# Kernel optimization log

Hardware: AMD Instinct MI355X
Metric: run time of the kernel (lower is better)

## Reference

```python
import jax, jax.numpy as jnp
import numpy as np

B, S, H = 32, 512, 768          # batch, encoder seq len, hidden size
W, G = 128, 4                   # max words per example, max tokens per word group
NH, HD, FF, NL, NLAB = 4, 192, 2048, 2, 6  # heads, head dim, ffn dim, layers, labels
EPS = 1e-5


def setup_inputs() -> dict:
    key = jax.random.key(0)
    ks = jax.random.split(key, 16)
    s = 0.02
    hidden = jax.random.normal(ks[0], (B, S, H), jnp.float32)
    word_token_idx = jax.random.randint(ks[1], (B, W, G), 0, S).astype(jnp.int32)
    glen = jax.random.randint(ks[2], (B, W), 1, G + 1)
    group_token_mask = jnp.arange(G)[None, None, :] < glen[:, :, None]  # [B,W,G] bool
    nwords = jax.random.randint(ks[3], (B,), W // 2, W + 1)
    word_valid = jnp.arange(W)[None, :] < nwords[:, None]               # [B,W] bool
    return {
        'hidden': hidden,
        'word_token_idx': word_token_idx,
        'group_token_mask': group_token_mask,
        'word_valid': word_valid,
        'qkv_w': jax.random.normal(ks[4], (NL, 3 * H, H), jnp.float32) * s,
        'qkv_b': jnp.zeros((NL, 3 * H), jnp.float32),
        'out_w': jax.random.normal(ks[5], (NL, H, H), jnp.float32) * s,
        'out_b': jnp.zeros((NL, H), jnp.float32),
        'ff1_w': jax.random.normal(ks[6], (NL, FF, H), jnp.float32) * s,
        'ff1_b': jnp.zeros((NL, FF), jnp.float32),
        'ff2_w': jax.random.normal(ks[7], (NL, H, FF), jnp.float32) * s,
        'ff2_b': jnp.zeros((NL, H), jnp.float32),
        'ln1_s': jnp.ones((NL, H), jnp.float32),
        'ln1_b': jnp.zeros((NL, H), jnp.float32),
        'ln2_s': jnp.ones((NL, H), jnp.float32),
        'ln2_b': jnp.zeros((NL, H), jnp.float32),
        'cls_w': jax.random.normal(ks[8], (NLAB, H), jnp.float32) * s,
        'cls_b': jnp.zeros((NLAB,), jnp.float32),
    }


def _ln(x, s, b):
    m = x.mean(-1, keepdims=True)
    v = ((x - m) ** 2).mean(-1, keepdims=True)
    return (x - m) * jax.lax.rsqrt(v + EPS) * s + b


def reference(hidden, word_token_idx, group_token_mask, word_valid,
              qkv_w, qkv_b, out_w, out_b, ff1_w, ff1_b, ff2_w, ff2_b,
              ln1_s, ln1_b, ln2_s, ln2_b, cls_w, cls_b):
    dt = hidden.dtype
    # ragged per-word gather + masked mean over each subword group: [B,W,G,H]
    gathered = jax.vmap(lambda h, i: h[i])(hidden, word_token_idx)
    gm = group_token_mask[..., None].astype(dt)
    wemb = (gathered * gm).sum(2) / jnp.maximum(gm.sum(2), 1.0)   # [B,W,H]
    # invalid (padded) words are zero, matching torch pad_sequence zero-padding
    wemb = wemb * word_valid[..., None].astype(dt)
    cls = hidden[:, 0, :]
    x = jnp.concatenate([cls[:, None, :], wemb], axis=1)          # [B, W+1, H]
    # key padding mask: True = padded position; CLS slot always valid
    pad = jnp.concatenate([jnp.zeros((B, 1), bool), ~word_valid], axis=1)
    neg = jnp.finfo(dt).min
    Lw = W + 1
    scale = 1.0 / np.sqrt(HD)
    for l in range(NL):  # 2 post-norm TransformerEncoder layers
        qkv = x @ qkv_w[l].T + qkv_b[l]
        q, k, v = jnp.split(qkv, 3, axis=-1)
        q = q.reshape(B, Lw, NH, HD).transpose(0, 2, 1, 3)
        k = k.reshape(B, Lw, NH, HD).transpose(0, 2, 1, 3)
        v = v.reshape(B, Lw, NH, HD).transpose(0, 2, 1, 3)
        scores = jnp.einsum('bhqd,bhkd->bhqk', q, k) * scale
        scores = jnp.where(pad[:, None, None, :], neg, scores)
        a = jax.nn.softmax(scores, axis=-1)
        ctx = jnp.einsum('bhqk,bhkd->bhqd', a, v).transpose(0, 2, 1, 3).reshape(B, Lw, H)
        attn = ctx @ out_w[l].T + out_b[l]
        x = _ln(x + attn, ln1_s[l], ln1_b[l])
        h1 = jax.nn.relu(x @ ff1_w[l].T + ff1_b[l])
        x = _ln(x + h1 @ ff2_w[l].T + ff2_b[l], ln2_s[l], ln2_b[l])
    pooled = x[:, 0, :]
    logits = pooled @ cls_w.T + cls_b
    return (logits, pooled)
```

## Files before the change

kernel.cpp:

```cpp
#include <hip/hip_runtime.h>
#include <hip/hip_bf16.h>
#include <math.h>

#define B_  32
#define S_  512
#define H_  768
#define W_  128
#define G_  4
#define LW  129
#define NH_ 4
#define HD_ 192
#define FF_ 2048
#define NL_ 2
#define NLAB_ 6
#define M_   (B_ * LW)
#define MPAD 4224
#define EPS_ 1e-5f
#define SCALE_ 0.07216878364870323f

#define TP 192
#define KP 160
#define KR 144
#define KLD 200

#define QW_SZ (3 * H_ * H_)
#define OW_SZ (H_ * H_)
#define F1_SZ (FF_ * H_)
#define F2_SZ (H_ * FF_)
#define WL_SZ (QW_SZ + OW_SZ + F1_SZ + F2_SZ)

typedef __bf16 bf16_8 __attribute__((ext_vector_type(8)));
typedef float  f32x4  __attribute__((ext_vector_type(4)));
typedef unsigned short ushort8_t __attribute__((ext_vector_type(8)));

__device__ __forceinline__ float b2f(unsigned short u) {
    union { unsigned int i; float f; } c; c.i = ((unsigned int)u) << 16; return c.f;
}
__device__ __forceinline__ unsigned short f2b(float f) {
    union { float f; unsigned int u; } c; c.f = f;
    unsigned int u = c.u;
    return (unsigned short)((u + 0x7FFFu + ((u >> 16) & 1u)) >> 16);
}

__device__ __forceinline__ float wave_sum(float v) {
#pragma unroll
    for (int off = 1; off < 64; off <<= 1) v += __shfl_xor(v, off, 64);
    return v;
}
__device__ __forceinline__ float block_sum(float v, float* red) {
    v = wave_sum(v);
    int wid = threadIdx.x >> 6, lane = threadIdx.x & 63;
    if (lane == 0) red[wid] = v;
    __syncthreads();
    float r = (red[0] + red[1]) + (red[2] + red[3]);
    __syncthreads();
    return r;
}

__global__ __launch_bounds__(256) void build_x_kernel(
    const float* __restrict__ hidden,
    const int*   __restrict__ wti,
    const int*   __restrict__ gmask,
    const int*   __restrict__ wvalid,
    unsigned short* __restrict__ xb)
{
    int t = blockIdx.x;
    int b = blockIdx.y;
    int tid = threadIdx.x;
    if (t >= LW) {
        int pr = M_ + b * 3 + (t - LW);
        size_t xo = (size_t)pr * H_;
#pragma unroll
        for (int i = 0; i < 3; i++) xb[xo + tid + i * 256] = 0;
        return;
    }
    size_t xo = ((size_t)b * LW + t) * H_;
    if (t == 0) {
        const float* src = hidden + (size_t)b * S_ * H_;
#pragma unroll
        for (int i = 0; i < 3; i++) xb[xo + tid + i * 256] = f2b(src[tid + i * 256]);
    } else {
        int w = t - 1;
        int valid = wvalid[b * W_ + w];
        int ids[G_]; float msk[G_]; float cnt = 0.f;
#pragma unroll
        for (int g = 0; g < G_; g++) {
            ids[g] = wti[(b * W_ + w) * G_ + g];
            msk[g] = (gmask[(b * W_ + w) * G_ + g] != 0) ? 1.f : 0.f;
            cnt += msk[g];
        }
        float inv = valid ? (1.f / fmaxf(cnt, 1.f)) : 0.f;
#pragma unroll
        for (int i = 0; i < 3; i++) {
            int c = tid + i * 256;
            float a = 0.f;
#pragma unroll
            for (int g = 0; g < G_; g++)
                a += msk[g] * hidden[((size_t)b * S_ + ids[g]) * H_ + c];
            xb[xo + c] = f2b(a * inv);
        }
    }
}

__global__ __launch_bounds__(256) void cvt_all_kernel(
    const float4* __restrict__ qw, const float4* __restrict__ ow,
    const float4* __restrict__ f1, const float4* __restrict__ f2,
    ushort4* __restrict__ dst)
{
    constexpr int WL4 = WL_SZ / 4;
    int i = blockIdx.x * 256 + threadIdx.x;
    int l = (i < WL4) ? 0 : 1;
    int j = i - l * WL4;
    float4 v;
    if (j < QW_SZ / 4)                          v = qw[l * (QW_SZ / 4) + j];
    else if (j < (QW_SZ + OW_SZ) / 4)           v = ow[l * (OW_SZ / 4) + j - QW_SZ / 4];
    else if (j < (QW_SZ + OW_SZ + F1_SZ) / 4)   v = f1[l * (F1_SZ / 4) + j - (QW_SZ + OW_SZ) / 4];
    else                                        v = f2[l * (F2_SZ / 4) + j - (QW_SZ + OW_SZ + F1_SZ) / 4];
    ushort4 o; o.x = f2b(v.x); o.y = f2b(v.y); o.z = f2b(v.z); o.w = f2b(v.w);
    dst[i] = o;
}

template <int BM, int BN, int BK, int RELU, int OUTBF, int SWZ>
__global__ __launch_bounds__(256) void gemm_mfma(
    const unsigned short* __restrict__ A,
    const unsigned short* __restrict__ Bw,
    const float* __restrict__ bias,
    void* __restrict__ Cout,
    int N, int K)
{
    constexpr int MI  = BM / 32;
    constexpr int NJ  = BN / 32;
    constexpr int CPR = BK / 8;
    constexpr int RPL = 2048 / BK;
    constexpr int SA  = BM * BK / 2048;
    constexpr int SB  = BN * BK / 2048;

    __shared__ __align__(16) unsigned short As[BM * BK];
    __shared__ __align__(16) unsigned short Bs[BN * BK];

    const int tid  = threadIdx.x;
    const int lane = tid & 63;
    const int wid  = tid >> 6;

    int bx = blockIdx.x, by = blockIdx.y;
    if (SWZ) {
        int nx = gridDim.x;
        int total = nx * gridDim.y;
        int id = by * nx + bx;
        int id2 = (id & 7) * (total >> 3) + (id >> 3);
        by = id2 / nx; bx = id2 - by * nx;
    }
    const int bm = by * BM;
    const int bn = bx * BN;

    const int wm = (wid & 1) * (BM / 2);
    const int wn = (wid >> 1) * (BN / 2);
    const int r  = lane & 15;
    const int q8 = lane >> 4;
    const int m8 = r & (CPR - 1);

    const int srow = tid / CPR;
    const int scol = (tid % CPR) ^ (srow & (CPR - 1));
    const unsigned short* Ag = A  + (size_t)(bm + srow) * K + scol * 8;
    const unsigned short* Bg = Bw + (size_t)(bn + srow) * K + scol * 8;

    const bf16_8* Af = (const bf16_8*)As;
    const bf16_8* Bf = (const bf16_8*)Bs;
    int arow[MI], brow[NJ];
#pragma unroll
    for (int i = 0; i < MI; i++) arow[i] = (wm + i * 16 + r) * CPR;
#pragma unroll
    for (int j = 0; j < NJ; j++) brow[j] = (wn + j * 16 + r) * CPR;

    f32x4 acc[MI][NJ];
#pragma unroll
    for (int i = 0; i < MI; i++)
#pragma unroll
        for (int j = 0; j < NJ; j++) acc[i][j] = (f32x4){0.f, 0.f, 0.f, 0.f};

    for (int k0 = 0; k0 < K; k0 += BK) {
#pragma unroll
        for (int s = 0; s < SA; s++)
            __builtin_amdgcn_global_load_lds(
                (const __attribute__((address_space(1))) void*)(Ag + (size_t)(s * RPL) * K + k0),
                (__attribute__((address_space(3))) void*)(As + s * 2048 + tid * 8), 16, 0, 0);
#pragma unroll
        for (int s = 0; s < SB; s++)
            __builtin_amdgcn_global_load_lds(
                (const __attribute__((address_space(1))) void*)(Bg + (size_t)(s * RPL) * K + k0),
                (__attribute__((address_space(3))) void*)(Bs + s * 2048 + tid * 8), 16, 0, 0);
        __syncthreads();
#pragma unroll
        for (int ks = 0; ks < BK / 32; ks++) {
            const int cc = (ks * 4 + q8) ^ m8;
            bf16_8 a[MI], b[NJ];
#pragma unroll
            for (int i = 0; i < MI; i++) a[i] = Af[arow[i] + cc];
#pragma unroll
            for (int j = 0; j < NJ; j++) b[j] = Bf[brow[j] + cc];
#pragma unroll
            for (int i = 0; i < MI; i++)
#pragma unroll
                for (int j = 0; j < NJ; j++)
                    acc[i][j] = __builtin_amdgcn_mfma_f32_16x16x32_bf16(a[i], b[j], acc[i][j], 0, 0, 0);
        }
        __syncthreads();
    }

    int col[NJ]; float bv[NJ];
#pragma unroll
    for (int j = 0; j < NJ; j++) { col[j] = bn + wn + j * 16 + r; bv[j] = bias[col[j]]; }
    const int row0 = bm + wm + ((lane >> 4) << 2);
#pragma unroll
    for (int i = 0; i < MI; i++) {
#pragma unroll
        for (int rg = 0; rg < 4; rg++) {
            size_t rowoff = (size_t)(row0 + i * 16 + rg) * N;
#pragma unroll
            for (int j = 0; j < NJ; j++) {
                float v = acc[i][j][rg] + bv[j];
                if (RELU) v = fmaxf(v, 0.f);
                if (OUTBF) ((unsigned short*)Cout)[rowoff + col[j]] = f2b(v);
                else       ((float*)Cout)[rowoff + col[j]] = v;
            }
        }
    }
}

__global__ __launch_bounds__(256) void vt_kernel(
    const unsigned short* __restrict__ qkv,
    unsigned short* __restrict__ vtb)
{
    __shared__ __align__(16) unsigned short Vs[KR * KLD];
    int bh = blockIdx.x;
    int b = bh >> 2, h = bh & 3;
    int tid = threadIdx.x;
    for (int c = tid; c < KR * 24; c += 256) {
        int t = c / 24, j = c - t * 24;
        ushort8_t v = (ushort8_t){0,0,0,0,0,0,0,0};
        if (t < LW)
            v = *(const ushort8_t*)(qkv + (size_t)(b * LW + t) * (3 * H_) + 2 * H_ + h * HD_ + j * 8);
        *(ushort8_t*)(&Vs[t * KLD + j * 8]) = v;
    }
    __syncthreads();
    size_t obase = (size_t)bh * (HD_ * KP);
    for (int c = tid; c < HD_ * (KP / 4); c += 256) {
        int d = c / (KP / 4), t0 = (c - d * (KP / 4)) * 4;
        ushort4 o;
        o.x = (t0 + 0 < KR) ? Vs[(t0 + 0) * KLD + d] : 0;
        o.y = (t0 + 1 < KR) ? Vs[(t0 + 1) * KLD + d] : 0;
        o.z = (t0 + 2 < KR) ? Vs[(t0 + 2) * KLD + d] : 0;
        o.w = (t0 + 3 < KR) ? Vs[(t0 + 3) * KLD + d] : 0;
        *(ushort4*)(&vtb[obase + (size_t)d * KP + t0]) = o;
    }
}

__global__ __launch_bounds__(256) void attn_score_kernel(
    const unsigned short* __restrict__ qkv,
    const int*            __restrict__ wvalid,
    unsigned short*       __restrict__ pb)
{
    __shared__ __align__(16) unsigned short Ks[KR * KLD];
    __shared__ float msk[KR];
    int mb = blockIdx.x;
    int bh = blockIdx.y;
    int b = bh >> 2, h = bh & 3;
    int tid = threadIdx.x, lane = tid & 63, wid = tid >> 6;
    int q = lane >> 4, r = lane & 15;

    for (int c = tid; c < KR * 24; c += 256) {
        int t = c / 24, j = c - t * 24;
        ushort8_t v = (ushort8_t){0,0,0,0,0,0,0,0};
        if (t < LW)
            v = *(const ushort8_t*)(qkv + (size_t)(b * LW + t) * (3 * H_) + H_ + h * HD_ + j * 8);
        *(ushort8_t*)(&Ks[t * KLD + j * 8]) = v;
    }
    if (tid < KR) {
        bool valid = (tid == 0) || (tid <= W_ && wvalid[b * W_ + tid - 1] != 0);
        msk[tid] = valid ? 0.f : -1e30f;
    }
    __syncthreads();

    const int qrow0 = mb * 64 + wid * 16;
    const unsigned short* Qp = qkv + ((size_t)(b * LW) + qrow0 + r) * (3 * H_) + h * HD_;

    f32x4 acc[9];
#pragma unroll
    for (int nt = 0; nt < 9; nt++) acc[nt] = (f32x4){0.f, 0.f, 0.f, 0.f};

    for (int ks = 0; ks < HD_ / 32; ks++) {
        bf16_8 a = *(const bf16_8*)(Qp + ks * 32 + q * 8);
#pragma unroll
        for (int nt = 0; nt < 9; nt++) {
            bf16_8 bfrag = *(const bf16_8*)(&Ks[(nt * 16 + r) * KLD + ks * 32 + q * 8]);
            acc[nt] = __builtin_amdgcn_mfma_f32_16x16x32_bf16(a, bfrag, acc[nt], 0, 0, 0);
        }
    }

    float mk[9];
#pragma unroll
    for (int nt = 0; nt < 9; nt++) mk[nt] = msk[nt * 16 + r];

    size_t pbase = (size_t)bh * (TP * KP);
#pragma unroll
    for (int rg = 0; rg < 4; rg++) {
        float v[9]; float mx = -1e30f;
#pragma unroll
        for (int nt = 0; nt < 9; nt++) { v[nt] = acc[nt][rg] * SCALE_ + mk[nt]; mx = fmaxf(mx, v[nt]); }
#pragma unroll
        for (int off = 1; off < 16; off <<= 1) mx = fmaxf(mx, __shfl_xor(mx, off, 64));
        float s = 0.f;
#pragma unroll
        for (int nt = 0; nt < 9; nt++) { v[nt] = __expf(v[nt] - mx); s += v[nt]; }
#pragma unroll
        for (int off = 1; off < 16; off <<= 1) s += __shfl_xor(s, off, 64);
        float inv = 1.f / s;
        int row = qrow0 + q * 4 + rg;
#pragma unroll
        for (int nt = 0; nt < 9; nt++)
            pb[pbase + (size_t)row * KP + nt * 16 + r] = f2b(v[nt] * inv);
        pb[pbase + (size_t)row * KP + KR + r] = 0;
    }
}

__global__ __launch_bounds__(256) void attn_pv_kernel(
    const unsigned short* __restrict__ pb,
    const unsigned short* __restrict__ vtb,
    unsigned short*       __restrict__ ctx)
{
    int mb = blockIdx.x;
    int bh = blockIdx.y;
    int b = bh >> 2, h = bh & 3;
    int tid = threadIdx.x, lane = tid & 63, wid = tid >> 6;
    int q = lane >> 4, r = lane & 15;
    int wm = (wid & 1) * 32, wn = (wid >> 1) * 96;

    size_t pbase = (size_t)bh * (TP * KP);
    size_t vbase = (size_t)bh * (HD_ * KP);

    f32x4 acc[2][6];
#pragma unroll
    for (int i = 0; i < 2; i++)
#pragma unroll
        for (int j = 0; j < 6; j++) acc[i][j] = (f32x4){0.f, 0.f, 0.f, 0.f};

    for (int ks = 0; ks < KP / 32; ks++) {
        bf16_8 a[2], bb[6];
#pragma unroll
        for (int i = 0; i < 2; i++)
            a[i] = *(const bf16_8*)(pb + pbase + (size_t)(mb * 64 + wm + i * 16 + r) * KP + ks * 32 + q * 8);
#pragma unroll
        for (int j = 0; j < 6; j++)
            bb[j] = *(const bf16_8*)(vtb + vbase + (size_t)(wn + j * 16 + r) * KP + ks * 32 + q * 8);
#pragma unroll
        for (int i = 0; i < 2; i++)
#pragma unroll
            for (int j = 0; j < 6; j++)
                acc[i][j] = __builtin_amdgcn_mfma_f32_16x16x32_bf16(a[i], bb[j], acc[i][j], 0, 0, 0);
    }

#pragma unroll
    for (int i = 0; i < 2; i++) {
#pragma unroll
        for (int rg = 0; rg < 4; rg++) {
            int t = mb * 64 + wm + i * 16 + q * 4 + rg;
            if (t < LW) {
                size_t rowoff = (size_t)(b * LW + t) * H_ + h * HD_;
#pragma unroll
                for (int j = 0; j < 6; j++)
                    ctx[rowoff + wn + j * 16 + r] = f2b(acc[i][j][rg]);
            }
        }
    }
}

__global__ __launch_bounds__(256) void add_ln_kernel(
    unsigned short* __restrict__ xb, const unsigned short* __restrict__ res,
    const float* __restrict__ sc, const float* __restrict__ bi)
{
    __shared__ float red[4];
    int row = blockIdx.x;
    int tid = threadIdx.x;
    size_t base = (size_t)row * H_;
    float v[3];
    float sum = 0.f;
#pragma unroll
    for (int i = 0; i < 3; i++) {
        int c = tid + i * 256;
        float t = b2f(xb[base + c]) + b2f(res[base + c]);
        v[i] = t; sum += t;
    }
    sum = block_sum(sum, red);
    float mean = sum * (1.f / H_);
    float var = 0.f;
#pragma unroll
    for (int i = 0; i < 3; i++) { float d = v[i] - mean; var += d * d; }
    var = block_sum(var, red);
    float inv = rsqrtf(var * (1.f / H_) + EPS_);
#pragma unroll
    for (int i = 0; i < 3; i++) {
        int c = tid + i * 256;
        xb[base + c] = f2b((v[i] - mean) * inv * sc[c] + bi[c]);
    }
}

__global__ __launch_bounds__(384) void cls_kernel(
    const unsigned short* __restrict__ xb,
    const float* __restrict__ cls_w, const float* __restrict__ cls_b,
    float* __restrict__ out)
{
    int b = blockIdx.x;
    int tid = threadIdx.x;
    const unsigned short* p = &xb[((size_t)b * LW) * H_];
    for (int c = tid; c < H_; c += 384) out[B_ * NLAB_ + b * H_ + c] = b2f(p[c]);
    int w = tid >> 6, lane = tid & 63;
    if (w < NLAB_) {
        const float* wv = &cls_w[w * H_];
        float acc = 0.f;
#pragma unroll
        for (int i = 0; i < H_ / 64; i++) {
            int c = lane + i * 64;
            acc += b2f(p[c]) * wv[c];
        }
        acc = wave_sum(acc);
        if (lane == 0) out[b * NLAB_ + w] = acc + cls_b[w];
    }
}

extern "C" void kernel_launch(void* const* d_in, const int* in_sizes, int n_in,
                              void* d_out, int out_size, void* d_ws, size_t ws_size,
                              hipStream_t stream) {
    const float* hidden = (const float*)d_in[0];
    const int*   wti    = (const int*)d_in[1];
    const int*   gmask  = (const int*)d_in[2];
    const int*   wvalid = (const int*)d_in[3];
    const float* qkv_w  = (const float*)d_in[4];
    const float* qkv_b  = (const float*)d_in[5];
    const float* out_w  = (const float*)d_in[6];
    const float* out_b  = (const float*)d_in[7];
    const float* ff1_w  = (const float*)d_in[8];
    const float* ff1_b  = (const float*)d_in[9];
    const float* ff2_w  = (const float*)d_in[10];
    const float* ff2_b  = (const float*)d_in[11];
    const float* ln1_s  = (const float*)d_in[12];
    const float* ln1_b  = (const float*)d_in[13];
    const float* ln2_s  = (const float*)d_in[14];
    const float* ln2_b  = (const float*)d_in[15];
    const float* cls_w  = (const float*)d_in[16];
    const float* cls_b  = (const float*)d_in[17];
    float* out = (float*)d_out;

    const size_t XSZ = (size_t)MPAD * H_;
    const size_t ASZ = (size_t)128 * TP * KP;
    unsigned short* U    = (unsigned short*)d_ws;
    unsigned short* vtb  = U;
    unsigned short* pb   = U + ASZ;
    unsigned short* tmpb = U;
    unsigned short* xb   = U + 2 * ASZ;
    unsigned short* ctxb = xb + XSZ;
    unsigned short* qkvb = ctxb + XSZ;
    unsigned short* wb   = qkvb + (size_t)MPAD * 3 * H_;

    build_x_kernel<<<dim3(LW + 3, B_), 256, 0, stream>>>(hidden, wti, gmask, wvalid, xb);
    cvt_all_kernel<<<2 * WL_SZ / 4 / 256, 256, 0, stream>>>(
        (const float4*)qkv_w, (const float4*)out_w,
        (const float4*)ff1_w, (const float4*)ff2_w, (ushort4*)wb);

    const int GM = MPAD / 64;
    for (int l = 0; l < NL_; l++) {
        unsigned short* wbl = wb + (size_t)l * WL_SZ;
        gemm_mfma<64, 128, 64, 0, 1, 0><<<dim3(3 * H_ / 128, GM), 256, 0, stream>>>(
            xb, wbl, qkv_b + (size_t)l * 3 * H_, qkvb, 3 * H_, H_);
        vt_kernel<<<128, 256, 0, stream>>>(qkvb, vtb);
        attn_score_kernel<<<dim3(3, 128), 256, 0, stream>>>(qkvb, wvalid, pb);
        attn_pv_kernel<<<dim3(3, 128), 256, 0, stream>>>(pb, vtb, ctxb);
        gemm_mfma<64, 64, 64, 0, 1, 1><<<dim3(H_ / 64, GM), 256, 0, stream>>>(
            ctxb, wbl + QW_SZ, out_b + (size_t)l * H_, tmpb, H_, H_);
        add_ln_kernel<<<M_, 256, 0, stream>>>(xb, tmpb,
            ln1_s + (size_t)l * H_, ln1_b + (size_t)l * H_);
        gemm_mfma<64, 128, 64, 1, 1, 1><<<dim3(FF_ / 128, GM), 256, 0, stream>>>(
            xb, wbl + QW_SZ + OW_SZ, ff1_b + (size_t)l * FF_, qkvb, FF_, H_);
        gemm_mfma<64, 64, 64, 0, 1, 1><<<dim3(H_ / 64, GM), 256, 0, stream>>>(
            qkvb, wbl + QW_SZ + OW_SZ + F1_SZ, ff2_b + (size_t)l * H_, tmpb, H_, FF_);
        add_ln_kernel<<<M_, 256, 0, stream>>>(xb, tmpb,
            ln2_s + (size_t)l * H_, ln2_b + (size_t)l * H_);
    }
    cls_kernel<<<B_, 384, 0, stream>>>(xb, cls_w, cls_b, out);
    (void)in_sizes; (void)n_in; (void)out_size; (void)ws_size;
}
```

Baseline: 419.1 us.

## Fuse attention score and PV kernels; use direct-load GEMM for out-projection

Merges the softmax-score kernel and the P·V kernel so the probability tile stays in shared memory instead of going through a global buffer, which removes one launch and a global write/read of P. Separately, the attention output projection switches to a new GEMM kernel that loads A and B fragments straight from global memory without LDS staging, using 128x32 tiles and a swizzled block order. The fused kernel uses more LDS per block, which may lower occupancy. The direct GEMM gives up shared-memory reuse of operands.

```diff
diff --git a/kernel.cpp b/kernel.cpp
--- a/kernel.cpp
+++ b/kernel.cpp
@@ -22,6 +22,7 @@
 #define KP 160
 #define KR 144
 #define KLD 200
+#define PLD 168
 
 #define QW_SZ (3 * H_ * H_)
 #define OW_SZ (H_ * H_)
@@ -227,6 +228,63 @@
     }
 }
 
+__global__ __launch_bounds__(256) void gemm_direct(
+    const unsigned short* __restrict__ A,
+    const unsigned short* __restrict__ Bw,
+    const float* __restrict__ bias,
+    unsigned short* __restrict__ Cout,
+    int N, int K)
+{
+    const int tid = threadIdx.x, lane = tid & 63, wid = tid >> 6;
+    int bx = blockIdx.x, by = blockIdx.y;
+    {
+        int nx = gridDim.x, total = nx * gridDim.y;
+        int id = by * nx + bx;
+        int id2 = (id & 7) * (total >> 3) + (id >> 3);
+        by = id2 / nx; bx = id2 - by * nx;
+    }
+    const int bm = by * 128 + wid * 32;
+    const int bn = bx * 32;
+    const int r = lane & 15, q8 = (lane >> 4) * 8;
+
+    const unsigned short* Ap = A  + (size_t)(bm + r) * K + q8;
+    const unsigned short* Bp = Bw + (size_t)(bn + r) * K + q8;
+    const size_t row16 = (size_t)16 * K;
+
+    f32x4 acc[2][2];
+#pragma unroll
+    for (int i = 0; i < 2; i++)
+#pragma unroll
+        for (int j = 0; j < 2; j++) acc[i][j] = (f32x4){0.f, 0.f, 0.f, 0.f};
+
+#pragma unroll 4
+    for (int k0 = 0; k0 < K; k0 += 32) {
+        bf16_8 a0 = *(const bf16_8*)(Ap + k0);
+        bf16_8 a1 = *(const bf16_8*)(Ap + row16 + k0);
+        bf16_8 b0 = *(const bf16_8*)(Bp + k0);
+        bf16_8 b1 = *(const bf16_8*)(Bp + row16 + k0);
+        acc[0][0] = __builtin_amdgcn_mfma_f32_16x16x32_bf16(a0, b0, acc[0][0], 0, 0, 0);
+        acc[0][1] = __builtin_amdgcn_mfma_f32_16x16x32_bf16(a0, b1, acc[0][1], 0, 0, 0);
+        acc[1][0] = __builtin_amdgcn_mfma_f32_16x16x32_bf16(a1, b0, acc[1][0], 0, 0, 0);
+        acc[1][1] = __builtin_amdgcn_mfma_f32_16x16x32_bf16(a1, b1, acc[1][1], 0, 0, 0);
+    }
+
+    int col[2]; float bv[2];
+#pragma unroll
+    for (int j = 0; j < 2; j++) { col[j] = bn + j * 16 + r; bv[j] = bias[col[j]]; }
+    const int row0 = bm + ((lane >> 4) << 2);
+#pragma unroll
+    for (int i = 0; i < 2; i++) {
+#pragma unroll
+        for (int rg = 0; rg < 4; rg++) {
+            size_t rowoff = (size_t)(row0 + i * 16 + rg) * N;
+#pragma unroll
+            for (int j = 0; j < 2; j++)
+                Cout[rowoff + col[j]] = f2b(acc[i][j][rg] + bv[j]);
+        }
+    }
+}
+
 __global__ __launch_bounds__(256) void vt_kernel(
     const unsigned short* __restrict__ qkv,
     unsigned short* __restrict__ vtb)
@@ -255,12 +313,14 @@
     }
 }
 
-__global__ __launch_bounds__(256) void attn_score_kernel(
+__global__ __launch_bounds__(256) void attn_fused_kernel(
     const unsigned short* __restrict__ qkv,
     const int*            __restrict__ wvalid,
-    unsigned short*       __restrict__ pb)
+    const unsigned short* __restrict__ vtb,
+    unsigned short*       __restrict__ ctx)
 {
     __shared__ __align__(16) unsigned short Ks[KR * KLD];
+    __shared__ __align__(16) unsigned short Ps[64 * PLD];
     __shared__ float msk[KR];
     int mb = blockIdx.x;
     int bh = blockIdx.y;
@@ -281,13 +341,12 @@
     }
     __syncthreads();
 
-    const int qrow0 = mb * 64 + wid * 16;
-    const unsigned short* Qp = qkv + ((size_t)(b * LW) + qrow0 + r) * (3 * H_) + h * HD_;
+    const int lrow0 = wid * 16;
+    const unsigned short* Qp = qkv + ((size_t)(b * LW) + mb * 64 + lrow0 + r) * (3 * H_) + h * HD_;
 
     f32x4 acc[9];
 #pragma unroll
     for (int nt = 0; nt < 9; nt++) acc[nt] = (f32x4){0.f, 0.f, 0.f, 0.f};
-
     for (int ks = 0; ks < HD_ / 32; ks++) {
         bf16_8 a = *(const bf16_8*)(Qp + ks * 32 + q * 8);
 #pragma unroll
@@ -296,12 +355,9 @@
             acc[nt] = __builtin_amdgcn_mfma_f32_16x16x32_bf16(a, bfrag, acc[nt], 0, 0, 0);
         }
     }
-
     float mk[9];
 #pragma unroll
     for (int nt = 0; nt < 9; nt++) mk[nt] = msk[nt * 16 + r];
-
-    size_t pbase = (size_t)bh * (TP * KP);
 #pragma unroll
     for (int rg = 0; rg < 4; rg++) {
         float v[9]; float mx = -1e30f;
@@ -315,40 +371,28 @@
 #pragma unroll
         for (int off = 1; off < 16; off <<= 1) s += __shfl_xor(s, off, 64);
         float inv = 1.f / s;
-        int row = qrow0 + q * 4 + rg;
+        int lr = lrow0 + q * 4 + rg;
 #pragma unroll
         for (int nt = 0; nt < 9; nt++)
-            pb[pbase + (size_t)row * KP + nt * 16 + r] = f2b(v[nt] * inv);
-        pb[pbase + (size_t)row * KP + KR + r] = 0;
-    }
-}
-
-__global__ __launch_bounds__(256) void attn_pv_kernel(
-    const unsigned short* __restrict__ pb,
-    const unsigned short* __restrict__ vtb,
-    unsigned short*       __restrict__ ctx)
-{
-    int mb = blockIdx.x;
-    int bh = blockIdx.y;
-    int b = bh >> 2, h = bh & 3;
-    int tid = threadIdx.x, lane = tid & 63, wid = tid >> 6;
-    int q = lane >> 4, r = lane & 15;
-    int wm = (wid & 1) * 32, wn = (wid >> 1) * 96;
-
-    size_t pbase = (size_t)bh * (TP * KP);
+            Ps[lr * PLD + nt * 16 + r] = f2b(v[nt] * inv);
+        Ps[lr * PLD + KR + r] = 0;
+    }
+    __syncthreads();
+
+    const int wm = (wid & 1) * 32, wn = (wid >> 1) * 96;
     size_t vbase = (size_t)bh * (HD_ * KP);
 
-    f32x4 acc[2][6];
+    f32x4 pacc[2][6];
 #pragma unroll
     for (int i = 0; i < 2; i++)
 #pragma unroll
-        for (int j = 0; j < 6; j++) acc[i][j] = (f32x4){0.f, 0.f, 0.f, 0.f};
+        for (int j = 0; j < 6; j++) pacc[i][j] = (f32x4){0.f, 0.f, 0.f, 0.f};
 
     for (int ks = 0; ks < KP / 32; ks++) {
         bf16_8 a[2], bb[6];
 #pragma unroll
         for (int i = 0; i < 2; i++)
-            a[i] = *(const bf16_8*)(pb + pbase + (size_t)(mb * 64 + wm + i * 16 + r) * KP + ks * 32 + q * 8);
+            a[i] = *(const bf16_8*)(&Ps[(wm + i * 16 + r) * PLD + ks * 32 + q * 8]);
 #pragma unroll
         for (int j = 0; j < 6; j++)
             bb[j] = *(const bf16_8*)(vtb + vbase + (size_t)(wn + j * 16 + r) * KP + ks * 32 + q * 8);
@@ -356,19 +400,19 @@
         for (int i = 0; i < 2; i++)
 #pragma unroll
             for (int j = 0; j < 6; j++)
-                acc[i][j] = __builtin_amdgcn_mfma_f32_16x16x32_bf16(a[i], bb[j], acc[i][j], 0, 0, 0);
+                pacc[i][j] = __builtin_amdgcn_mfma_f32_16x16x32_bf16(a[i], bb[j], pacc[i][j], 0, 0, 0);
     }
 
 #pragma unroll
     for (int i = 0; i < 2; i++) {
 #pragma unroll
         for (int rg = 0; rg < 4; rg++) {
-            int t = mb * 64 + wm + i * 16 + q * 4 + rg;
-            if (t < LW) {
-                size_t rowoff = (size_t)(b * LW + t) * H_ + h * HD_;
+            int tl = mb * 64 + wm + i * 16 + q * 4 + rg;
+            if (tl < LW) {
+                size_t rowoff = (size_t)(b * LW + tl) * H_ + h * HD_;
 #pragma unroll
                 for (int j = 0; j < 6; j++)
-                    ctx[rowoff + wn + j * 16 + r] = f2b(acc[i][j][rg]);
+                    ctx[rowoff + wn + j * 16 + r] = f2b(pacc[i][j][rg]);
             }
         }
     }
@@ -454,9 +498,8 @@
     const size_t ASZ = (size_t)128 * TP * KP;
     unsigned short* U    = (unsigned short*)d_ws;
     unsigned short* vtb  = U;
-    unsigned short* pb   = U + ASZ;
     unsigned short* tmpb = U;
-    unsigned short* xb   = U + 2 * ASZ;
+    unsigned short* xb   = U + ASZ;
     unsigned short* ctxb = xb + XSZ;
     unsigned short* qkvb = ctxb + XSZ;
     unsigned short* wb   = qkvb + (size_t)MPAD * 3 * H_;
@@ -472,9 +515,8 @@
         gemm_mfma<64, 128, 64, 0, 1, 0><<<dim3(3 * H_ / 128, GM), 256, 0, stream>>>(
             xb, wbl, qkv_b + (size_t)l * 3 * H_, qkvb, 3 * H_, H_);
         vt_kernel<<<128, 256, 0, stream>>>(qkvb, vtb);
-        attn_score_kernel<<<dim3(3, 128), 256, 0, stream>>>(qkvb, wvalid, pb);
-        attn_pv_kernel<<<dim3(3, 128), 256, 0, stream>>>(pb, vtb, ctxb);
-        gemm_mfma<64, 64, 64, 0, 1, 1><<<dim3(H_ / 64, GM), 256, 0, stream>>>(
+        attn_fused_kernel<<<dim3(3, 128), 256, 0, stream>>>(qkvb, wvalid, vtb, ctxb);
+        gemm_direct<<<dim3(H_ / 32, MPAD / 128), 256, 0, stream>>>(
             ctxb, wbl + QW_SZ, out_b + (size_t)l * H_, tmpb, H_, H_);
         add_ln_kernel<<<M_, 256, 0, stream>>>(xb, tmpb,
             ln1_s + (size_t)l * H_, ln1_b + (size_t)l * H_);
```

Result: slower. 476.1 us (+13.6%).
